# Kernel tuning notes

Hardware: AMD Instinct MI355X
Metric: run time of the kernel (lower is better)

## Reference

```python
import jax, jax.numpy as jnp
import numpy as np

NUM_HEADS = 16
BLOCK_SIZE = 64


def setup_inputs() -> dict:
    key = jax.random.key(0)
    ks = jax.random.split(key, 5)
    B, S, C = 2, 2047, 1024
    return {
        "x": jax.random.normal(ks[0], (B, S, C), dtype=jnp.float32),
        "global_token": jax.random.normal(ks[1], (1, 1, C), dtype=jnp.float32),
        "qkv_w": jax.random.normal(ks[2], (3 * C, C), dtype=jnp.float32) * 0.02,
        "proj_w": jax.random.normal(ks[3], (C, C), dtype=jnp.float32) * 0.02,
        "proj_b": jax.random.normal(ks[4], (C,), dtype=jnp.float32) * 0.02,
    }


def reference(x, global_token, qkv_w, proj_w, proj_b):
    B, S, C = x.shape
    H = NUM_HEADS
    D = C // H
    scale = D ** -0.5
    # prepend global token -> N = S + 1
    g = jnp.broadcast_to(global_token, (B, 1, C))
    xg = jnp.concatenate([g, x], axis=1)
    N = S + 1
    # fused qkv projection (torch Linear: x @ W^T)
    qkv = (xg @ qkv_w.T).reshape(B, N, 3, H, D)
    qkv = jnp.transpose(qkv, (2, 0, 3, 1, 4))  # [3, B, H, N, D]
    q, k, v = qkv[0], qkv[1], qkv[2]
    # block-causal mask: query t sees key j iff block(j) <= block(t)
    blk = jnp.arange(N) // BLOCK_SIZE
    mask = blk[:, None] >= blk[None, :]  # [N, N]
    attn = jnp.einsum("bhqd,bhkd->bhqk", q, k) * scale
    attn = jnp.where(mask[None, None], attn, -jnp.inf)
    attn = jax.nn.softmax(attn, axis=-1)
    out = jnp.einsum("bhqk,bhkd->bhqd", attn, v)
    out = jnp.transpose(out, (0, 2, 1, 3)).reshape(B, N, C)
    out = out[:, 1:, :]  # drop global token
    return out @ proj_w.T + proj_b
```

## Files before the change

### kernel.cpp

```cpp
#include <hip/hip_runtime.h>
#include <math.h>

typedef _Float16 h16;
typedef _Float16 half8 __attribute__((ext_vector_type(8)));
typedef _Float16 half4 __attribute__((ext_vector_type(4)));
typedef float f32x4 __attribute__((ext_vector_type(4)));

#define NB 2
#define NS 2047
#define NC 1024
#define NN 2048
#define NH 16
#define ND 64

__device__ __forceinline__ void gl_lds16(const h16* g, h16* l) {
  __builtin_amdgcn_global_load_lds((const __attribute__((address_space(1))) void*)g,
                                   (__attribute__((address_space(3))) void*)l, 16, 0, 0);
}
__device__ __forceinline__ f32x4 mfma32(half8 a, half8 b, f32x4 c) {
  return __builtin_amdgcn_mfma_f32_16x16x32_f16(a, b, c, 0, 0, 0);
}
__device__ __forceinline__ f32x4 mfma16x(half4 a, half4 b, f32x4 c) {
  return __builtin_amdgcn_mfma_f32_16x16x16f16(a, b, c, 0, 0, 0);
}
#define WAITVM4 __builtin_amdgcn_s_waitcnt(0x0F74)
#define WAITLG0 __builtin_amdgcn_s_waitcnt(0xC07F)

__global__ __launch_bounds__(256) void cast_xg_k(
    const float* __restrict__ x, const float* __restrict__ g, h16* __restrict__ out) {
  size_t i = ((size_t)blockIdx.x * 256 + threadIdx.x) * 16;
  const int c = (int)(i & (NC - 1));
  const int n = (int)((i >> 10) & (NN - 1));
  const int b = (int)(i >> 21);
  const float* src = (n == 0) ? (g + c) : (x + ((size_t)b * NS + (n - 1)) * NC + c);
  h16 tmp[16];
#pragma unroll
  for (int j = 0; j < 4; ++j) {
    float4 f = ((const float4*)src)[j];
    tmp[4 * j + 0] = (h16)f.x; tmp[4 * j + 1] = (h16)f.y;
    tmp[4 * j + 2] = (h16)f.z; tmp[4 * j + 3] = (h16)f.w;
  }
  *(half8*)(out + i) = *(half8*)&tmp[0];
  *(half8*)(out + i + 8) = *(half8*)&tmp[8];
}

__global__ __launch_bounds__(256) void cast_w_k(
    const float* __restrict__ qw, const float* __restrict__ pw, h16* __restrict__ out) {
  size_t i = ((size_t)blockIdx.x * 256 + threadIdx.x) * 8;
  const float* src = (i < (size_t)3 * NC * NC) ? (qw + i) : (pw + (i - (size_t)3 * NC * NC));
  float4 f0 = ((const float4*)src)[0];
  float4 f1 = ((const float4*)src)[1];
  h16 tmp[8];
  tmp[0] = (h16)f0.x; tmp[1] = (h16)f0.y; tmp[2] = (h16)f0.z; tmp[3] = (h16)f0.w;
  tmp[4] = (h16)f1.x; tmp[5] = (h16)f1.y; tmp[6] = (h16)f1.z; tmp[7] = (h16)f1.w;
  *(half8*)(out + i) = *(half8*)&tmp[0];
}

__global__ __launch_bounds__(256) void gemm_qkv_h(
    const h16* __restrict__ A, const h16* __restrict__ W, h16* __restrict__ out) {
  __shared__ h16 As[128 * 64];
  __shared__ h16 Bs[128 * 64];
  const int tid = threadIdx.x;
  const int m0 = blockIdx.y * 128, j0 = blockIdx.x * 128;
  const int wid = tid >> 6, lane = tid & 63, l15 = lane & 15, quad = lane >> 4;
  const int rl = lane >> 3, cp = lane & 7, csw = cp ^ rl;
  const h16* ag = A + (size_t)(m0 + wid * 32 + rl) * NC + csw * 8;
  const h16* bg = W + (size_t)(j0 + wid * 32 + rl) * NC + csw * 8;
  f32x4 acc[2][8];
#pragma unroll
  for (int rt = 0; rt < 2; ++rt)
#pragma unroll
    for (int ct = 0; ct < 8; ++ct) acc[rt][ct] = (f32x4){0.f, 0.f, 0.f, 0.f};

  for (int k0 = 0; k0 < NC; k0 += 64) {
    __syncthreads();
#pragma unroll
    for (int i = 0; i < 4; ++i) {
      gl_lds16(ag + (size_t)i * 8 * NC + k0, &As[(wid * 32 + i * 8) * 64]);
      gl_lds16(bg + (size_t)i * 8 * NC + k0, &Bs[(wid * 32 + i * 8) * 64]);
    }
    __syncthreads();
#pragma unroll
    for (int ks = 0; ks < 2; ++ks) {
      const int p0 = ((ks * 4 + quad) ^ (l15 & 7)) * 8;
      half8 af0 = *(const half8*)&As[(wid * 32 + l15) * 64 + p0];
      half8 af1 = *(const half8*)&As[(wid * 32 + 16 + l15) * 64 + p0];
#pragma unroll
      for (int ct = 0; ct < 8; ++ct) {
        half8 bf = *(const half8*)&Bs[(ct * 16 + l15) * 64 + p0];
        acc[0][ct] = mfma32(af0, bf, acc[0][ct]);
        acc[1][ct] = mfma32(af1, bf, acc[1][ct]);
      }
    }
  }
#pragma unroll
  for (int rt = 0; rt < 2; ++rt)
#pragma unroll
    for (int ct = 0; ct < 8; ++ct)
#pragma unroll
      for (int r = 0; r < 4; ++r) {
        const int mm = m0 + wid * 32 + rt * 16 + quad * 4 + r;
        const int jj = j0 + ct * 16 + l15;
        out[(size_t)mm * (3 * NC) + jj] = (h16)acc[rt][ct][r];
      }
}

__global__ __launch_bounds__(256) void vtrans_k(
    const h16* __restrict__ qkvh, h16* __restrict__ vT) {
  __shared__ h16 ts[64 * 72];
  const int kb = blockIdx.x, h = blockIdx.y, b = blockIdx.z;
  const int t = threadIdx.x;
  const int key = t >> 2, co = (t & 3) * 16;
  const h16* src = qkvh + (size_t)(b * NN + kb * 64 + key) * (3 * NC) + 2 * NC + h * ND + co;
  half8 v0 = *(const half8*)src;
  half8 v1 = *(const half8*)(src + 8);
  *(half8*)&ts[key * 72 + co] = v0;
  *(half8*)&ts[key * 72 + co + 8] = v1;
  __syncthreads();
  const int d = t >> 2, ko = (t & 3) * 16;
  h16 buf[16];
#pragma unroll
  for (int i = 0; i < 16; ++i) buf[i] = ts[(ko + i) * 72 + d];
  h16* dst = vT + ((size_t)(b * NH + h) * ND + d) * NN + kb * 64 + ko;
  *(half8*)dst = *(half8*)&buf[0];
  *(half8*)(dst + 8) = *(half8*)&buf[8];
}

__global__ __launch_bounds__(256, 3) void attn_h(
    const h16* __restrict__ qkvh, const h16* __restrict__ vT, h16* __restrict__ outp) {
  __shared__ h16 K0[4][1024];
  __shared__ h16 V0[4][1024];
  __shared__ h16 K1[4][1024];
  __shared__ h16 V1[4][1024];
  __shared__ float RED[2 * 64 * 36];
  __shared__ float DEN[4 * 64];
  const int bx = blockIdx.x;
  const int qb = 31 - (bx >> 5);
  const int bh = bx & 31;
  const int b = bh >> 4, h = bh & 15;
  const int tid = threadIdx.x, w = tid >> 6, lane = tid & 63;
  const int l15 = lane & 15, quad = lane >> 4;

  half8 bq[4][2];
#pragma unroll
  for (int nt = 0; nt < 4; ++nt) {
    const h16* qp = qkvh + (size_t)(b * NN + qb * 64 + nt * 16 + l15) * (3 * NC) + h * ND + quad * 8;
    half8 t0 = *(const half8*)qp;
    half8 t1 = *(const half8*)(qp + 32);
    bq[nt][0] = t0 * (h16)0.125f;
    bq[nt][1] = t1 * (h16)0.125f;
  }

  const int rl = lane >> 3, csw = (lane & 7) ^ rl;
  const h16* ksrc = qkvh + ((size_t)(b * NN + w * 16 + rl) * 3 + 1) * NC + h * ND + csw * 8;
  const h16* vsrc = vT + ((size_t)(b * NH + h) * ND + (lane >> 1)) * NN + w * 16 + (lane & 1) * 8;

  const int ka0 = l15 * 64 + ((quad) ^ (l15 & 7)) * 8;
  const int ka1 = l15 * 64 + ((quad + 4) ^ (l15 & 7)) * 8;

  f32x4 o[4][4];
  float den[4] = {0.f, 0.f, 0.f, 0.f};
#pragma unroll
  for (int mt = 0; mt < 4; ++mt)
#pragma unroll
    for (int nt = 0; nt < 4; ++nt) o[mt][nt] = (f32x4){0.f, 0.f, 0.f, 0.f};

#define STAGE(Kd, Vd, kb)                                 \
  {                                                       \
    const h16* kp_ = ksrc + (size_t)(kb) * (64 * 3 * NC); \
    const h16* vp_ = vsrc + (kb) * 64;                    \
    gl_lds16(kp_, &Kd[w][0]);                             \
    gl_lds16(kp_ + (size_t)8 * 3 * NC, &Kd[w][512]);      \
    gl_lds16(vp_, &Vd[w][0]);                             \
    gl_lds16(vp_ + (size_t)32 * NN, &Vd[w][512]);         \
  }

#define COMPUTE(Kd, Vd)                                                       \
  {                                                                           \
    half8 kf0 = *(const half8*)&Kd[w][ka0];                                   \
    half8 kf1 = *(const half8*)&Kd[w][ka1];                                   \
    half4 vf[4];                                                              \
    _Pragma("unroll") for (int mt = 0; mt < 4; ++mt)                          \
        vf[mt] = *(const half4*)&Vd[w][(mt * 16 + l15) * 16 + quad * 4];      \
    _Pragma("unroll") for (int nt = 0; nt < 4; ++nt) {                        \
      f32x4 s = (f32x4){0.f, 0.f, 0.f, 0.f};                                  \
      s = mfma32(kf0, bq[nt][0], s);                                          \
      s = mfma32(kf1, bq[nt][1], s);                                          \
      float e0 = __expf(s[0]), e1 = __expf(s[1]);                             \
      float e2 = __expf(s[2]), e3 = __expf(s[3]);                             \
      den[nt] += (e0 + e1) + (e2 + e3);                                       \
      int2 pi;                                                                \
      pi.x = __builtin_bit_cast(int, __builtin_amdgcn_cvt_pkrtz(e0, e1));     \
      pi.y = __builtin_bit_cast(int, __builtin_amdgcn_cvt_pkrtz(e2, e3));     \
      half4 p = __builtin_bit_cast(half4, pi);                                \
      _Pragma("unroll") for (int mt = 0; mt < 4; ++mt)                        \
          o[mt][nt] = mfma16x(vf[mt], p, o[mt][nt]);                          \
    }                                                                         \
  }

  STAGE(K0, V0, 0);
  {
    const int k1 = (qb >= 1) ? 1 : 0;
    STAGE(K1, V1, k1);
  }
  for (int kb = 0; kb <= qb; kb += 2) {
    WAITVM4;
    __builtin_amdgcn_wave_barrier();
    COMPUTE(K0, V0);
    WAITLG0;
    __builtin_amdgcn_wave_barrier();
    {
      const int nk = (kb + 2 <= qb) ? kb + 2 : kb;
      STAGE(K0, V0, nk);
    }
    if (kb + 1 <= qb) {
      WAITVM4;
      __builtin_amdgcn_wave_barrier();
      COMPUTE(K1, V1);
      WAITLG0;
      __builtin_amdgcn_wave_barrier();
      {
        const int nk = (kb + 3 <= qb) ? kb + 3 : kb + 1;
        STAGE(K1, V1, nk);
      }
    }
  }

#pragma unroll
  for (int nt = 0; nt < 4; ++nt) {
    den[nt] += __shfl_xor(den[nt], 16);
    den[nt] += __shfl_xor(den[nt], 32);
  }
  __syncthreads();
  if (quad == 0) {
#pragma unroll
    for (int nt = 0; nt < 4; ++nt) DEN[w * 64 + nt * 16 + l15] = den[nt];
  }
#pragma unroll
  for (int r = 0; r < 2; ++r) {
    if (r) __syncthreads();
    if (w < 2) {
#pragma unroll
      for (int mt2 = 0; mt2 < 2; ++mt2)
#pragma unroll
        for (int nt = 0; nt < 4; ++nt)
          *(f32x4*)&RED[(w * 64 + nt * 16 + l15) * 36 + mt2 * 16 + quad * 4] =
              o[r * 2 + mt2][nt];
    }
    __syncthreads();
    if (w >= 2) {
#pragma unroll
      for (int mt2 = 0; mt2 < 2; ++mt2)
#pragma unroll
        for (int nt = 0; nt < 4; ++nt) {
          float* p = &RED[((w - 2) * 64 + nt * 16 + l15) * 36 + mt2 * 16 + quad * 4];
          f32x4 t = *(f32x4*)p;
          *(f32x4*)p = t + o[r * 2 + mt2][nt];
        }
    }
    __syncthreads();
    {
      const int q = w * 16 + l15;
      const float dt = DEN[q] + DEN[64 + q] + DEN[128 + q] + DEN[192 + q];
      const float inv = 1.f / dt;
      f32x4 x0 = *(const f32x4*)&RED[(0 * 64 + q) * 36 + quad * 8];
      f32x4 x1 = *(const f32x4*)&RED[(0 * 64 + q) * 36 + quad * 8 + 4];
      f32x4 y0 = *(const f32x4*)&RED[(1 * 64 + q) * 36 + quad * 8];
      f32x4 y1 = *(const f32x4*)&RED[(1 * 64 + q) * 36 + quad * 8 + 4];
      x0 += y0;
      x1 += y1;
      int4 pk;
      pk.x = __builtin_bit_cast(int, __builtin_amdgcn_cvt_pkrtz(x0[0] * inv, x0[1] * inv));
      pk.y = __builtin_bit_cast(int, __builtin_amdgcn_cvt_pkrtz(x0[2] * inv, x0[3] * inv));
      pk.z = __builtin_bit_cast(int, __builtin_amdgcn_cvt_pkrtz(x1[0] * inv, x1[1] * inv));
      pk.w = __builtin_bit_cast(int, __builtin_amdgcn_cvt_pkrtz(x1[2] * inv, x1[3] * inv));
      h16* op = outp + (size_t)(b * NN + qb * 64 + q) * NC + h * ND + r * 32 + quad * 8;
      *(half8*)op = __builtin_bit_cast(half8, pk);
    }
  }
#undef STAGE
#undef COMPUTE
}

__global__ __launch_bounds__(256) void gemm_proj_h(
    const h16* __restrict__ Ah, const h16* __restrict__ W,
    const float* __restrict__ bias, float* __restrict__ out) {
  __shared__ h16 As[64 * 64];
  __shared__ h16 Bs[128 * 64];
  const int tid = threadIdx.x;
  const int m0 = blockIdx.y * 64, j0 = blockIdx.x * 128;
  const int wid = tid >> 6, lane = tid & 63, l15 = lane & 15, quad = lane >> 4;
  const int rl = lane >> 3, csw = (lane & 7) ^ rl;
  const h16* ag[2];
#pragma unroll
  for (int i = 0; i < 2; ++i) {
    int m = m0 + wid * 16 + i * 8 + rl;
    if (m > NB * NS - 1) m = NB * NS - 1;
    const int bb = (m >= NS) ? 1 : 0;
    ag[i] = Ah + (size_t)(bb * NN + m - bb * NS + 1) * NC + csw * 8;
  }
  const h16* bg = W + (size_t)(j0 + wid * 32 + rl) * NC + csw * 8;
  f32x4 acc[8];
#pragma unroll
  for (int ct = 0; ct < 8; ++ct) acc[ct] = (f32x4){0.f, 0.f, 0.f, 0.f};

  for (int k0 = 0; k0 < NC; k0 += 64) {
    __syncthreads();
    gl_lds16(ag[0] + k0, &As[(wid * 16) * 64]);
    gl_lds16(ag[1] + k0, &As[(wid * 16 + 8) * 64]);
#pragma unroll
    for (int i = 0; i < 4; ++i)
      gl_lds16(bg + (size_t)i * 8 * NC + k0, &Bs[(wid * 32 + i * 8) * 64]);
    __syncthreads();
#pragma unroll
    for (int ks = 0; ks < 2; ++ks) {
      const int p0 = ((ks * 4 + quad) ^ (l15 & 7)) * 8;
      half8 af = *(const half8*)&As[(wid * 16 + l15) * 64 + p0];
#pragma unroll
      for (int ct = 0; ct < 8; ++ct) {
        half8 bf = *(const half8*)&Bs[(ct * 16 + l15) * 64 + p0];
        acc[ct] = mfma32(af, bf, acc[ct]);
      }
    }
  }
#pragma unroll
  for (int ct = 0; ct < 8; ++ct) {
    const float bv = bias[j0 + ct * 16 + l15];
#pragma unroll
    for (int r = 0; r < 4; ++r) {
      const int mm = m0 + wid * 16 + quad * 4 + r;
      if (mm < NB * NS)
        out[(size_t)mm * NC + j0 + ct * 16 + l15] = acc[ct][r] + bv;
    }
  }
}

extern "C" void kernel_launch(void* const* d_in, const int* in_sizes, int n_in,
                              void* d_out, int out_size, void* d_ws, size_t ws_size,
                              hipStream_t stream) {
  const float* x = (const float*)d_in[0];
  const float* g = (const float*)d_in[1];
  const float* qkv_w = (const float*)d_in[2];
  const float* proj_w = (const float*)d_in[3];
  const float* proj_b = (const float*)d_in[4];
  float* out = (float*)d_out;

  h16* xgh  = (h16*)d_ws;
  h16* w3h  = xgh + (size_t)NB * NN * NC;
  h16* wph  = w3h + (size_t)3 * NC * NC;
  h16* qkvh = wph + (size_t)NC * NC;
  h16* vTh  = qkvh + (size_t)NB * NN * 3 * NC;
  h16* attnh = vTh + (size_t)NB * NH * ND * NN;

  cast_xg_k<<<dim3(1024), 256, 0, stream>>>(x, g, xgh);
  cast_w_k<<<dim3(2048), 256, 0, stream>>>(qkv_w, proj_w, w3h);
  gemm_qkv_h<<<dim3(24, 32), 256, 0, stream>>>(xgh, w3h, qkvh);
  vtrans_k<<<dim3(32, NH, NB), 256, 0, stream>>>(qkvh, vTh);
  attn_h<<<dim3(1024), 256, 0, stream>>>(qkvh, vTh, attnh);
  gemm_proj_h<<<dim3(8, 64), 256, 0, stream>>>(attnh, wph, proj_b, out);
}
```

Before: 183.2 us.

## Pack K/V into per-head contiguous layouts and load attention operands directly to registers

The pre-pass now writes K into a contiguous per-(batch,head) buffer and V into a fragment-ordered layout, so each attention lane can load its MFMA operands straight from global memory into registers. The double-buffered global-to-LDS staging, with its waitcnt and barrier choreography, is replaced by a simple one-block-ahead register prefetch. The two fp32-to-fp16 cast kernels are merged into one launch. The pack kernel writes an extra K copy to global memory, and attention now relies on cache hits and register prefetch rather than LDS buffering to hide latency.

```diff
diff --git a/kernel.cpp b/kernel.cpp
--- a/kernel.cpp
+++ b/kernel.cpp
@@ -23,31 +23,21 @@
 __device__ __forceinline__ f32x4 mfma16x(half4 a, half4 b, f32x4 c) {
   return __builtin_amdgcn_mfma_f32_16x16x16f16(a, b, c, 0, 0, 0);
 }
-#define WAITVM4 __builtin_amdgcn_s_waitcnt(0x0F74)
-#define WAITLG0 __builtin_amdgcn_s_waitcnt(0xC07F)
-
-__global__ __launch_bounds__(256) void cast_xg_k(
-    const float* __restrict__ x, const float* __restrict__ g, h16* __restrict__ out) {
-  size_t i = ((size_t)blockIdx.x * 256 + threadIdx.x) * 16;
-  const int c = (int)(i & (NC - 1));
-  const int n = (int)((i >> 10) & (NN - 1));
-  const int b = (int)(i >> 21);
-  const float* src = (n == 0) ? (g + c) : (x + ((size_t)b * NS + (n - 1)) * NC + c);
-  h16 tmp[16];
-#pragma unroll
-  for (int j = 0; j < 4; ++j) {
-    float4 f = ((const float4*)src)[j];
-    tmp[4 * j + 0] = (h16)f.x; tmp[4 * j + 1] = (h16)f.y;
-    tmp[4 * j + 2] = (h16)f.z; tmp[4 * j + 3] = (h16)f.w;
-  }
-  *(half8*)(out + i) = *(half8*)&tmp[0];
-  *(half8*)(out + i + 8) = *(half8*)&tmp[8];
-}
-
-__global__ __launch_bounds__(256) void cast_w_k(
+
+__global__ __launch_bounds__(256) void cast_all_k(
+    const float* __restrict__ x, const float* __restrict__ g,
     const float* __restrict__ qw, const float* __restrict__ pw, h16* __restrict__ out) {
-  size_t i = ((size_t)blockIdx.x * 256 + threadIdx.x) * 8;
-  const float* src = (i < (size_t)3 * NC * NC) ? (qw + i) : (pw + (i - (size_t)3 * NC * NC));
+  const size_t i = ((size_t)blockIdx.x * 256 + threadIdx.x) * 8;
+  const float* src;
+  if (i < (size_t)NB * NN * NC) {
+    const int c = (int)(i & (NC - 1));
+    const int n = (int)((i >> 10) & (NN - 1));
+    const int b = (int)(i >> 21);
+    src = (n == 0) ? (g + c) : (x + ((size_t)b * NS + (n - 1)) * NC + c);
+  } else {
+    const size_t j = i - (size_t)NB * NN * NC;
+    src = (j < (size_t)3 * NC * NC) ? (qw + j) : (pw + (j - (size_t)3 * NC * NC));
+  }
   float4 f0 = ((const float4*)src)[0];
   float4 f1 = ((const float4*)src)[1];
   h16 tmp[8];
@@ -105,33 +95,44 @@
       }
 }
 
-__global__ __launch_bounds__(256) void vtrans_k(
-    const h16* __restrict__ qkvh, h16* __restrict__ vT) {
+__global__ __launch_bounds__(256) void kvpack_k(
+    const h16* __restrict__ qkvh, h16* __restrict__ kP, h16* __restrict__ vP) {
   __shared__ h16 ts[64 * 72];
   const int kb = blockIdx.x, h = blockIdx.y, b = blockIdx.z;
+  const int bh = b * NH + h;
   const int t = threadIdx.x;
-  const int key = t >> 2, co = (t & 3) * 16;
-  const h16* src = qkvh + (size_t)(b * NN + kb * 64 + key) * (3 * NC) + 2 * NC + h * ND + co;
-  half8 v0 = *(const half8*)src;
-  half8 v1 = *(const half8*)(src + 8);
-  *(half8*)&ts[key * 72 + co] = v0;
-  *(half8*)&ts[key * 72 + co + 8] = v1;
+  {
+    const int r = t >> 2, c = (t & 3) * 16;
+    const h16* src = qkvh + ((size_t)(b * NN + kb * 64 + r) * 3 + 1) * NC + h * ND + c;
+    half8 k0 = *(const half8*)src;
+    half8 k1 = *(const half8*)(src + 8);
+    h16* dst = kP + ((size_t)bh * NN + kb * 64 + r) * ND + c;
+    *(half8*)dst = k0;
+    *(half8*)(dst + 8) = k1;
+  }
+  {
+    const int key = t >> 2, co = (t & 3) * 16;
+    const h16* src = qkvh + ((size_t)(b * NN + kb * 64 + key) * 3 + 2) * NC + h * ND + co;
+    half8 v0 = *(const half8*)src;
+    half8 v1 = *(const half8*)(src + 8);
+    *(half8*)&ts[key * 72 + co] = v0;
+    *(half8*)&ts[key * 72 + co + 8] = v1;
+  }
   __syncthreads();
-  const int d = t >> 2, ko = (t & 3) * 16;
-  h16 buf[16];
-#pragma unroll
-  for (int i = 0; i < 16; ++i) buf[i] = ts[(ko + i) * 72 + d];
-  h16* dst = vT + ((size_t)(b * NH + h) * ND + d) * NN + kb * 64 + ko;
-  *(half8*)dst = *(half8*)&buf[0];
-  *(half8*)(dst + 8) = *(half8*)&buf[8];
+  {
+    const int w = t >> 6, d = t & 63;
+    h16 buf[16];
+#pragma unroll
+    for (int kk = 0; kk < 16; ++kk) buf[kk] = ts[(w * 16 + kk) * 72 + d];
+    h16* dst = vP + ((size_t)(bh * 32 + kb) * 4 + w) * 1024 + d * 16;
+    *(half8*)dst = *(half8*)&buf[0];
+    *(half8*)(dst + 8) = *(half8*)&buf[8];
+  }
 }
 
 __global__ __launch_bounds__(256, 3) void attn_h(
-    const h16* __restrict__ qkvh, const h16* __restrict__ vT, h16* __restrict__ outp) {
-  __shared__ h16 K0[4][1024];
-  __shared__ h16 V0[4][1024];
-  __shared__ h16 K1[4][1024];
-  __shared__ h16 V1[4][1024];
+    const h16* __restrict__ qkvh, const h16* __restrict__ kP,
+    const h16* __restrict__ vP, h16* __restrict__ outp) {
   __shared__ float RED[2 * 64 * 36];
   __shared__ float DEN[4 * 64];
   const int bx = blockIdx.x;
@@ -145,18 +146,11 @@
 #pragma unroll
   for (int nt = 0; nt < 4; ++nt) {
     const h16* qp = qkvh + (size_t)(b * NN + qb * 64 + nt * 16 + l15) * (3 * NC) + h * ND + quad * 8;
-    half8 t0 = *(const half8*)qp;
-    half8 t1 = *(const half8*)(qp + 32);
-    bq[nt][0] = t0 * (h16)0.125f;
-    bq[nt][1] = t1 * (h16)0.125f;
-  }
-
-  const int rl = lane >> 3, csw = (lane & 7) ^ rl;
-  const h16* ksrc = qkvh + ((size_t)(b * NN + w * 16 + rl) * 3 + 1) * NC + h * ND + csw * 8;
-  const h16* vsrc = vT + ((size_t)(b * NH + h) * ND + (lane >> 1)) * NN + w * 16 + (lane & 1) * 8;
-
-  const int ka0 = l15 * 64 + ((quad) ^ (l15 & 7)) * 8;
-  const int ka1 = l15 * 64 + ((quad + 4) ^ (l15 & 7)) * 8;
+    bq[nt][0] = (*(const half8*)qp) * (h16)0.125f;
+    bq[nt][1] = (*(const half8*)(qp + 32)) * (h16)0.125f;
+  }
+  const h16* kbase = kP + ((size_t)bh * NN + w * 16 + l15) * ND + quad * 8;
+  const h16* vbase = vP + ((size_t)bh * 32 * 4 + w) * 1024 + l15 * 16 + quad * 4;
 
   f32x4 o[4][4];
   float den[4] = {0.f, 0.f, 0.f, 0.f};
@@ -165,65 +159,42 @@
 #pragma unroll
     for (int nt = 0; nt < 4; ++nt) o[mt][nt] = (f32x4){0.f, 0.f, 0.f, 0.f};
 
-#define STAGE(Kd, Vd, kb)                                 \
-  {                                                       \
-    const h16* kp_ = ksrc + (size_t)(kb) * (64 * 3 * NC); \
-    const h16* vp_ = vsrc + (kb) * 64;                    \
-    gl_lds16(kp_, &Kd[w][0]);                             \
-    gl_lds16(kp_ + (size_t)8 * 3 * NC, &Kd[w][512]);      \
-    gl_lds16(vp_, &Vd[w][0]);                             \
-    gl_lds16(vp_ + (size_t)32 * NN, &Vd[w][512]);         \
-  }
-
-#define COMPUTE(Kd, Vd)                                                       \
-  {                                                                           \
-    half8 kf0 = *(const half8*)&Kd[w][ka0];                                   \
-    half8 kf1 = *(const half8*)&Kd[w][ka1];                                   \
-    half4 vf[4];                                                              \
-    _Pragma("unroll") for (int mt = 0; mt < 4; ++mt)                          \
-        vf[mt] = *(const half4*)&Vd[w][(mt * 16 + l15) * 16 + quad * 4];      \
-    _Pragma("unroll") for (int nt = 0; nt < 4; ++nt) {                        \
-      f32x4 s = (f32x4){0.f, 0.f, 0.f, 0.f};                                  \
-      s = mfma32(kf0, bq[nt][0], s);                                          \
-      s = mfma32(kf1, bq[nt][1], s);                                          \
-      float e0 = __expf(s[0]), e1 = __expf(s[1]);                             \
-      float e2 = __expf(s[2]), e3 = __expf(s[3]);                             \
-      den[nt] += (e0 + e1) + (e2 + e3);                                       \
-      int2 pi;                                                                \
-      pi.x = __builtin_bit_cast(int, __builtin_amdgcn_cvt_pkrtz(e0, e1));     \
-      pi.y = __builtin_bit_cast(int, __builtin_amdgcn_cvt_pkrtz(e2, e3));     \
-      half4 p = __builtin_bit_cast(half4, pi);                                \
-      _Pragma("unroll") for (int mt = 0; mt < 4; ++mt)                        \
-          o[mt][nt] = mfma16x(vf[mt], p, o[mt][nt]);                          \
-    }                                                                         \
-  }
-
-  STAGE(K0, V0, 0);
-  {
-    const int k1 = (qb >= 1) ? 1 : 0;
-    STAGE(K1, V1, k1);
-  }
-  for (int kb = 0; kb <= qb; kb += 2) {
-    WAITVM4;
-    __builtin_amdgcn_wave_barrier();
-    COMPUTE(K0, V0);
-    WAITLG0;
-    __builtin_amdgcn_wave_barrier();
-    {
-      const int nk = (kb + 2 <= qb) ? kb + 2 : kb;
-      STAGE(K0, V0, nk);
-    }
-    if (kb + 1 <= qb) {
-      WAITVM4;
-      __builtin_amdgcn_wave_barrier();
-      COMPUTE(K1, V1);
-      WAITLG0;
-      __builtin_amdgcn_wave_barrier();
-      {
-        const int nk = (kb + 3 <= qb) ? kb + 3 : kb + 1;
-        STAGE(K1, V1, nk);
-      }
-    }
+  half8 kf0 = *(const half8*)kbase;
+  half8 kf1 = *(const half8*)(kbase + 32);
+  half4 vf0 = *(const half4*)(vbase);
+  half4 vf1 = *(const half4*)(vbase + 256);
+  half4 vf2 = *(const half4*)(vbase + 512);
+  half4 vf3 = *(const half4*)(vbase + 768);
+
+  for (int kb = 0; kb <= qb; ++kb) {
+    const int nkb = (kb < qb) ? kb + 1 : kb;
+    const h16* kn = kbase + (size_t)nkb * 64 * ND;
+    const h16* vn = vbase + (size_t)nkb * 4096;
+    half8 nk0 = *(const half8*)kn;
+    half8 nk1 = *(const half8*)(kn + 32);
+    half4 nv0 = *(const half4*)(vn);
+    half4 nv1 = *(const half4*)(vn + 256);
+    half4 nv2 = *(const half4*)(vn + 512);
+    half4 nv3 = *(const half4*)(vn + 768);
+#pragma unroll
+    for (int nt = 0; nt < 4; ++nt) {
+      f32x4 s = (f32x4){0.f, 0.f, 0.f, 0.f};
+      s = mfma32(kf0, bq[nt][0], s);
+      s = mfma32(kf1, bq[nt][1], s);
+      float e0 = __expf(s[0]), e1 = __expf(s[1]);
+      float e2 = __expf(s[2]), e3 = __expf(s[3]);
+      den[nt] += (e0 + e1) + (e2 + e3);
+      int2 pi;
+      pi.x = __builtin_bit_cast(int, __builtin_amdgcn_cvt_pkrtz(e0, e1));
+      pi.y = __builtin_bit_cast(int, __builtin_amdgcn_cvt_pkrtz(e2, e3));
+      half4 p = __builtin_bit_cast(half4, pi);
+      o[0][nt] = mfma16x(vf0, p, o[0][nt]);
+      o[1][nt] = mfma16x(vf1, p, o[1][nt]);
+      o[2][nt] = mfma16x(vf2, p, o[2][nt]);
+      o[3][nt] = mfma16x(vf3, p, o[3][nt]);
+    }
+    kf0 = nk0; kf1 = nk1;
+    vf0 = nv0; vf1 = nv1; vf2 = nv2; vf3 = nv3;
   }
 
 #pragma unroll
@@ -278,8 +249,6 @@
       *(half8*)op = __builtin_bit_cast(half8, pk);
     }
   }
-#undef STAGE
-#undef COMPUTE
 }
 
 __global__ __launch_bounds__(256) void gemm_proj_h(
@@ -349,13 +318,13 @@
   h16* w3h  = xgh + (size_t)NB * NN * NC;
   h16* wph  = w3h + (size_t)3 * NC * NC;
   h16* qkvh = wph + (size_t)NC * NC;
-  h16* vTh  = qkvh + (size_t)NB * NN * 3 * NC;
-  h16* attnh = vTh + (size_t)NB * NH * ND * NN;
-
-  cast_xg_k<<<dim3(1024), 256, 0, stream>>>(x, g, xgh);
-  cast_w_k<<<dim3(2048), 256, 0, stream>>>(qkv_w, proj_w, w3h);
+  h16* kPb  = qkvh + (size_t)NB * NN * 3 * NC;
+  h16* vPb  = kPb + (size_t)NB * NH * NN * ND;
+  h16* attnh = vPb + (size_t)NB * NH * NN * ND;
+
+  cast_all_k<<<dim3(4096), 256, 0, stream>>>(x, g, qkv_w, proj_w, xgh);
   gemm_qkv_h<<<dim3(24, 32), 256, 0, stream>>>(xgh, w3h, qkvh);
-  vtrans_k<<<dim3(32, NH, NB), 256, 0, stream>>>(qkvh, vTh);
-  attn_h<<<dim3(1024), 256, 0, stream>>>(qkvh, vTh, attnh);
+  kvpack_k<<<dim3(32, NH, NB), 256, 0, stream>>>(qkvh, kPb, vPb);
+  attn_h<<<dim3(1024), 256, 0, stream>>>(qkvh, kPb, vPb, attnh);
   gemm_proj_h<<<dim3(8, 64), 256, 0, stream>>>(attnh, wph, proj_b, out);
 }
```

Result: faster. 179.2 us (-2.2%).
